# Kernel optimization log

Measured on AMD Instinct MI355X. Metric: run time of the kernel, lower is better.

The kernel has to match this reference:

```python
import jax, jax.numpy as jnp
import numpy as np
from jax import lax

# static config matching init_kwargs
H, W = 128, 128
THETA_RES, RHO_RES = 1.0, 1.0
C_IN, C_OUT = 64, 64
A = int(np.round(180.0 / THETA_RES))            # num angle bins = 180
R = int(np.ceil(np.sqrt(H * H + W * W) / RHO_RES))  # num rho bins = 182


def _make_rho_idx():
    # rho bin index for every (angle, pixel); pixels flattened h-major (h*W + w)
    th = np.arange(A, dtype=np.float64) * THETA_RES * np.pi / 180.0
    hh, ww = np.meshgrid(np.arange(H), np.arange(W), indexing='ij')
    xs = (ww - W / 2.0).ravel()
    ys = (hh - H / 2.0).ravel()
    r = np.round((xs[None, :] * np.cos(th)[:, None]
                  + ys[None, :] * np.sin(th)[:, None]) / RHO_RES).astype(np.int32)
    r = r + R // 2
    return np.clip(r, 0, R - 1)  # [A, H*W] int32


def dht(x, rho_idx):
    # Hough scatter: [N,C,H,W] -> [N,C,A,R]
    N, C, h, w = x.shape
    xf = x.reshape(N * C, h * w).T  # [HW, NC]

    def step(_, idx_a):
        acc = jax.ops.segment_sum(xf, idx_a, num_segments=R)  # [R, NC]
        return None, acc

    _, ht = lax.scan(step, None, rho_idx)       # [A, R, NC]
    return ht.transpose(2, 0, 1).reshape(N, C, A, R)


def idht(ht, rho_idx):
    # inverse Hough gather (transpose of dht): [N,C,A,R] -> [N,C,H,W]
    N, C, a, r = ht.shape
    hf = ht.reshape(N * C, a, r).transpose(1, 0, 2)  # [A, NC, R]

    def step(acc, args):
        ht_a, idx_a = args
        return acc + ht_a[:, idx_a], None  # gather along rho -> [NC, HW]

    acc0 = jnp.zeros((N * C, H * W), ht.dtype)
    acc, _ = lax.scan(step, acc0, (hf, rho_idx))
    return acc.reshape(N, C, H, W)


def conv91_relu(x, w, b, groups):
    # Conv2d kernel (9,1), padding (4,0), stride 1 + ReLU
    y = lax.conv_general_dilated(x, w, (1, 1), [(4, 4), (0, 0)],
                                 dimension_numbers=('NCHW', 'OIHW', 'NCHW'),
                                 feature_group_count=groups)
    return jax.nn.relu(y + b[None, :, None, None])


def setup_inputs():
    key = jax.random.key(0)
    ks = jax.random.split(key, 7)
    N = 4
    x = jax.random.normal(ks[0], (N, C_IN, H, W), dtype=jnp.float32)
    s1 = 1.0 / np.sqrt(9.0)
    s2 = 1.0 / np.sqrt(9.0 * C_IN)
    w1 = jax.random.normal(ks[1], (C_IN, 1, 9, 1), jnp.float32) * s1
    b1 = jax.random.normal(ks[2], (C_IN,), jnp.float32) * 0.01
    w2 = jax.random.normal(ks[3], (C_IN, C_IN, 9, 1), jnp.float32) * s2
    b2 = jax.random.normal(ks[4], (C_IN,), jnp.float32) * 0.01
    w3 = jax.random.normal(ks[5], (C_OUT, C_IN, 9, 1), jnp.float32) * s2
    b3 = jax.random.normal(ks[6], (C_OUT,), jnp.float32) * 0.01
    rho_idx = jnp.asarray(_make_rho_idx())  # [A, H*W] int32, precomputed buffer
    return {"x": x, "rho_idx": rho_idx, "w1": w1, "b1": b1,
            "w2": w2, "b2": b2, "w3": w3, "b3": b3}


def reference(x, rho_idx, w1, b1, w2, b2, w3, b3):
    out = dht(x, rho_idx)                       # [N,C,A,R]
    out = conv91_relu(out, w1, b1, groups=C_IN) # grouped (9,1) conv
    out = conv91_relu(out, w2, b2, groups=1)
    out = conv91_relu(out, w3, b3, groups=1)
    return idht(out, rho_idx)                   # [N,C_OUT,H,W]
```

## Files before the change

### kernel.cpp

```cpp
#include <hip/hip_runtime.h>

typedef unsigned short ushort_t;
typedef __attribute__((ext_vector_type(8))) short short8;
typedef __attribute__((ext_vector_type(4))) float float4v;

#define HW 16384
#define A_BINS 180
#define R_BINS 182
#define AP 188
#define CCH 64
#define NB 4
#define NC 256
#define MROWS (A_BINS * R_BINS)
#define MPROWS (AP * R_BINS)

static __device__ __forceinline__ float b2f(ushort_t u) {
    union { unsigned u32; float f; } c; c.u32 = ((unsigned)u) << 16; return c.f;
}
static __device__ __forceinline__ float u2f(unsigned u) {
    union { unsigned u32; float f; } c; c.u32 = u; return c.f;
}
static __device__ __forceinline__ ushort_t f2b(float f) {
    union { float f; unsigned u; } c; c.f = f;
    unsigned r = c.u + 0x7fffu + ((c.u >> 16) & 1u);
    return (ushort_t)(r >> 16);
}
static __device__ __forceinline__ float4v cvt4(uint2 u) {
    return (float4v){u2f(u.x << 16), u2f(u.x & 0xffff0000u),
                     u2f(u.y << 16), u2f(u.y & 0xffff0000u)};
}

__global__ __launch_bounds__(256) void k_transpose(const float* __restrict__ x,
                                                   ushort_t* __restrict__ xT) {
    __shared__ float tile[64][65];
    int t = threadIdx.x, lane = t & 63, g = t >> 6;
    int pBase = blockIdx.x * 64;
    int ncBase = blockIdx.y * 64;
#pragma unroll
    for (int i = 0; i < 16; ++i) {
        int ncl = g + i * 4;
        tile[ncl][lane] = x[(size_t)(ncBase + ncl) * HW + pBase + lane];
    }
    __syncthreads();
#pragma unroll
    for (int i = 0; i < 16; ++i) {
        int pl = g + i * 4;
        xT[(size_t)(pBase + pl) * 256 + ncBase + lane] = f2b(tile[lane][pl]);
    }
}

__global__ __launch_bounds__(256) void k_setup(ushort_t* __restrict__ ht0,
                                               ushort_t* __restrict__ bufA,
                                               ushort_t* __restrict__ bufB,
                                               const float* __restrict__ w2,
                                               const float* __restrict__ w3,
                                               ushort_t* __restrict__ w2b,
                                               ushort_t* __restrict__ w3b) {
    int blk = blockIdx.x, t = threadIdx.x;
    if (blk < 24) {
        int b = blk >> 3, j = blk & 7;
        int ap = (j < 4) ? j : (184 + (j - 4));
        ushort_t* base = (b == 0 ? ht0 : (b == 1 ? bufA : bufB));
        uint4* p = (uint4*)(base + (size_t)ap * (R_BINS * NC));
        int n16 = R_BINS * NC / 8;
        for (int i = t; i < n16; i += 256) p[i] = (uint4){0, 0, 0, 0};
        return;
    }
    int rep = blk - 24;
    const float* w = (rep >= 144) ? w3 : w2;
    ushort_t* wb = (rep >= 144) ? w3b : w2b;
    int idx = (rep % 144) * 256 + t;
    int j = idx & 7;
    int lane = (idx >> 3) & 63;
    int cot = (idx >> 9) & 3;
    int h = (idx >> 11) & 1;
    int k = idx >> 12;
    int co = cot * 16 + (lane & 15);
    int ci = h * 32 + (lane >> 4) * 8 + j;
    wb[idx] = f2b(w[(co * 64 + ci) * 9 + k]);
}

__global__ __launch_bounds__(256) void k_csr(const int* __restrict__ rho,
                                             int* __restrict__ offs,
                                             ushort_t* __restrict__ plist) {
    __shared__ int hist[4][R_BINS];
    __shared__ int tot[R_BINS];
    __shared__ int offl[R_BINS + 1];
    __shared__ int cur[4][R_BINS];
    __shared__ ushort_t sp[HW];
    int a = blockIdx.x, t = threadIdx.x, lane = t & 63, wv = t >> 6;
    for (int i = t; i < 4 * R_BINS; i += 256) ((int*)hist)[i] = 0;
    __syncthreads();
    const int* rA = rho + (size_t)a * HW;
#pragma unroll 4
    for (int i = 0; i < 64; ++i) {
        int r = rA[t + i * 256];
        atomicAdd(&hist[wv][r], 1);
    }
    __syncthreads();
    if (t < R_BINS) tot[t] = hist[0][t] + hist[1][t] + hist[2][t] + hist[3][t];
    __syncthreads();
    if (wv == 0) {
        int b0 = lane * 3;
        int c0 = (b0     < R_BINS) ? tot[b0]     : 0;
        int c1 = (b0 + 1 < R_BINS) ? tot[b0 + 1] : 0;
        int c2 = (b0 + 2 < R_BINS) ? tot[b0 + 2] : 0;
        int sum = c0 + c1 + c2, inc = sum;
#pragma unroll
        for (int d = 1; d < 64; d <<= 1) {
            int vv = __shfl_up(inc, d);
            if (lane >= d) inc += vv;
        }
        int excl = inc - sum;
        if (b0     < R_BINS) offl[b0]     = excl;
        if (b0 + 1 < R_BINS) offl[b0 + 1] = excl + c0;
        if (b0 + 2 < R_BINS) offl[b0 + 2] = excl + c0 + c1;
        if (lane == 63) offl[R_BINS] = inc;
    }
    __syncthreads();
    if (t < R_BINS) {
        int b = offl[t];
        cur[0][t] = b; b += hist[0][t];
        cur[1][t] = b; b += hist[1][t];
        cur[2][t] = b; b += hist[2][t];
        cur[3][t] = b;
    }
    if (t <= R_BINS) offs[a * (R_BINS + 1) + t] = offl[t];
    __syncthreads();
#pragma unroll 4
    for (int i = 0; i < 64; ++i) {
        int p = t + i * 256;
        int r = rA[p];
        int pos = atomicAdd(&cur[wv][r], 1);
        sp[pos] = (ushort_t)p;
    }
    __syncthreads();
    const uint4* spv = (const uint4*)sp;
    uint4* plv = (uint4*)(plist + (size_t)a * HW);
    for (int i = t; i < HW / 8; i += 256) plv[i] = spv[i];
}

__global__ __launch_bounds__(256, 4) void k_dht_g4(const ushort_t* __restrict__ xT,
                                                   const int* __restrict__ offs,
                                                   const ushort_t* __restrict__ plist,
                                                   ushort_t* __restrict__ ht0) {
    int a = blockIdx.x, part = blockIdx.y;
    int t = threadIdx.x, lane = t & 63, wv = t >> 6;
    int wslot = part * 4 + wv;
    int lo4 = lane << 2;
    const uint*  plw = (const uint*)(plist + (size_t)a * HW);
    const uint4* plq = (const uint4*)plw;
    const int* offA = offs + a * (R_BINS + 1);
    size_t obase = (size_t)(a + 4) * (R_BINS * NC);
    for (int r = wslot; r < R_BINS; r += 64) {
        int off = __builtin_amdgcn_readfirstlane(offA[r]);
        int end = __builtin_amdgcn_readfirstlane(offA[r + 1]);
        float4v acc = (float4v){0.f, 0.f, 0.f, 0.f};
        int j = off;
        while (j < end && (j & 7)) {
            unsigned up = __builtin_amdgcn_readfirstlane(plw[j >> 1]);
            unsigned p = (j & 1) ? (up >> 16) : (up & 0xffffu);
            acc += cvt4(*(const uint2*)(xT + ((size_t)p << 8) + lo4));
            ++j;
        }
        if (j + 16 <= end) {
            uint4 q0 = plq[j >> 3];
            uint4 q1 = plq[(j >> 3) + 1];
            for (; j + 16 <= end; ) {
                int jn = j + 16;
                uint4 n0, n1;
                bool more = (jn + 16 <= end);
                if (more) {
                    n0 = plq[jn >> 3];
                    n1 = plq[(jn >> 3) + 1];
                }
                unsigned w0 = __builtin_amdgcn_readfirstlane(q0.x);
                unsigned w1 = __builtin_amdgcn_readfirstlane(q0.y);
                unsigned w2 = __builtin_amdgcn_readfirstlane(q0.z);
                unsigned w3 = __builtin_amdgcn_readfirstlane(q0.w);
                unsigned w4 = __builtin_amdgcn_readfirstlane(q1.x);
                unsigned w5 = __builtin_amdgcn_readfirstlane(q1.y);
                unsigned w6 = __builtin_amdgcn_readfirstlane(q1.z);
                unsigned w7 = __builtin_amdgcn_readfirstlane(q1.w);
                uint2 u0 = *(const uint2*)(xT + ((size_t)(w0 & 0xffffu) << 8) + lo4);
                uint2 u1 = *(const uint2*)(xT + ((size_t)(w0 >> 16)     << 8) + lo4);
                uint2 u2 = *(const uint2*)(xT + ((size_t)(w1 & 0xffffu) << 8) + lo4);
                uint2 u3 = *(const uint2*)(xT + ((size_t)(w1 >> 16)     << 8) + lo4);
                uint2 u4 = *(const uint2*)(xT + ((size_t)(w2 & 0xffffu) << 8) + lo4);
                uint2 u5 = *(const uint2*)(xT + ((size_t)(w2 >> 16)     << 8) + lo4);
                uint2 u6 = *(const uint2*)(xT + ((size_t)(w3 & 0xffffu) << 8) + lo4);
                uint2 u7 = *(const uint2*)(xT + ((size_t)(w3 >> 16)     << 8) + lo4);
                uint2 u8 = *(const uint2*)(xT + ((size_t)(w4 & 0xffffu) << 8) + lo4);
                uint2 u9 = *(const uint2*)(xT + ((size_t)(w4 >> 16)     << 8) + lo4);
                uint2 ua = *(const uint2*)(xT + ((size_t)(w5 & 0xffffu) << 8) + lo4);
                uint2 ub = *(const uint2*)(xT + ((size_t)(w5 >> 16)     << 8) + lo4);
                uint2 uc = *(const uint2*)(xT + ((size_t)(w6 & 0xffffu) << 8) + lo4);
                uint2 ud = *(const uint2*)(xT + ((size_t)(w6 >> 16)     << 8) + lo4);
                uint2 ue = *(const uint2*)(xT + ((size_t)(w7 & 0xffffu) << 8) + lo4);
                uint2 uf = *(const uint2*)(xT + ((size_t)(w7 >> 16)     << 8) + lo4);
                acc += cvt4(u0); acc += cvt4(u1); acc += cvt4(u2); acc += cvt4(u3);
                acc += cvt4(u4); acc += cvt4(u5); acc += cvt4(u6); acc += cvt4(u7);
                acc += cvt4(u8); acc += cvt4(u9); acc += cvt4(ua); acc += cvt4(ub);
                acc += cvt4(uc); acc += cvt4(ud); acc += cvt4(ue); acc += cvt4(uf);
                q0 = n0; q1 = n1; j = jn;
            }
        }
        for (; j + 8 <= end; j += 8) {
            uint4 q0 = plq[j >> 3];
            unsigned w0 = __builtin_amdgcn_readfirstlane(q0.x);
            unsigned w1 = __builtin_amdgcn_readfirstlane(q0.y);
            unsigned w2 = __builtin_amdgcn_readfirstlane(q0.z);
            unsigned w3 = __builtin_amdgcn_readfirstlane(q0.w);
            uint2 u0 = *(const uint2*)(xT + ((size_t)(w0 & 0xffffu) << 8) + lo4);
            uint2 u1 = *(const uint2*)(xT + ((size_t)(w0 >> 16)     << 8) + lo4);
            uint2 u2 = *(const uint2*)(xT + ((size_t)(w1 & 0xffffu) << 8) + lo4);
            uint2 u3 = *(const uint2*)(xT + ((size_t)(w1 >> 16)     << 8) + lo4);
            uint2 u4 = *(const uint2*)(xT + ((size_t)(w2 & 0xffffu) << 8) + lo4);
            uint2 u5 = *(const uint2*)(xT + ((size_t)(w2 >> 16)     << 8) + lo4);
            uint2 u6 = *(const uint2*)(xT + ((size_t)(w3 & 0xffffu) << 8) + lo4);
            uint2 u7 = *(const uint2*)(xT + ((size_t)(w3 >> 16)     << 8) + lo4);
            acc += cvt4(u0); acc += cvt4(u1); acc += cvt4(u2); acc += cvt4(u3);
            acc += cvt4(u4); acc += cvt4(u5); acc += cvt4(u6); acc += cvt4(u7);
        }
        while (j < end) {
            unsigned up = __builtin_amdgcn_readfirstlane(plw[j >> 1]);
            unsigned p = (j & 1) ? (up >> 16) : (up & 0xffffu);
            acc += cvt4(*(const uint2*)(xT + ((size_t)p << 8) + lo4));
            ++j;
        }
        unsigned lo = (unsigned)f2b(acc.x) | ((unsigned)f2b(acc.y) << 16);
        unsigned hi = (unsigned)f2b(acc.z) | ((unsigned)f2b(acc.w) << 16);
        *(uint2*)(ht0 + obase + (size_t)r * NC + lo4) = (uint2){lo, hi};
    }
}

__global__ __launch_bounds__(256) void k_conv1(const ushort_t* __restrict__ ht0,
                                               const float* __restrict__ w1,
                                               const float* __restrict__ b1,
                                               ushort_t* __restrict__ bufA) {
    int t = threadIdx.x, c = t & 63;
    int r = blockIdx.x;
    int a0 = blockIdx.y * 30;
    float wr[9];
#pragma unroll
    for (int k = 0; k < 9; ++k) wr[k] = w1[c * 9 + k];
    float bb = b1[c];
    const ushort_t* ip = ht0 + ((size_t)a0 * R_BINS + r) * NC + t;
    float v[38];
#pragma unroll
    for (int j = 0; j < 38; ++j) v[j] = b2f(ip[(size_t)j * (R_BINS * NC)]);
    ushort_t* op = bufA + ((size_t)(a0 + 4) * R_BINS + r) * NC + t;
#pragma unroll
    for (int i = 0; i < 30; ++i) {
        float s = bb;
#pragma unroll
        for (int k = 0; k < 9; ++k) s = fmaf(v[i + k], wr[k], s);
        op[(size_t)i * (R_BINS * NC)] = f2b(fmaxf(s, 0.f));
    }
}

__global__ __launch_bounds__(256) void k_gemm(const ushort_t* __restrict__ in,
                                              const ushort_t* __restrict__ wb,
                                              const float* __restrict__ bias,
                                              ushort_t* __restrict__ out,
                                              int outRowOff) {
    __shared__ ushort_t Bs[36864];
    int t = threadIdx.x, lane = t & 63, wv = t >> 6;
    {
        const uint4* src = (const uint4*)wb;
        uint4* dst = (uint4*)Bs;
        for (int i = t; i < 36864 / 8; i += 256) dst[i] = src[i];
    }
    __syncthreads();
    int m = lane & 15, q = lane >> 4;
    int n = blockIdx.y;
    int rowBase = blockIdx.x * 256 + wv * 64;
    const ushort_t* inN = in + n * 64;
    size_t rof[4];
#pragma unroll
    for (int tl = 0; tl < 4; ++tl) {
        int row = rowBase + tl * 16 + m;
        int rowc = row < MROWS ? row : (MROWS - 1);
        rof[tl] = (size_t)rowc * NC;
    }
    float4v acc[4][4];
#pragma unroll
    for (int tl = 0; tl < 4; ++tl)
#pragma unroll
        for (int i = 0; i < 4; ++i) acc[tl][i] = (float4v){0.f, 0.f, 0.f, 0.f};

#pragma unroll
    for (int k = 0; k < 9; ++k) {
#pragma unroll
        for (int h = 0; h < 2; ++h) {
            const ushort_t* base = inN + (size_t)k * (R_BINS * NC) + h * 32 + q * 8;
            short8 af0 = *(const short8*)(base + rof[0]);
            short8 af1 = *(const short8*)(base + rof[1]);
            short8 af2 = *(const short8*)(base + rof[2]);
            short8 af3 = *(const short8*)(base + rof[3]);
            const ushort_t* bl = Bs + (size_t)((k * 2 + h) * 4) * 512 + lane * 8;
            short8 b0 = *(const short8*)(bl);
            short8 b1v = *(const short8*)(bl + 512);
            short8 b2v = *(const short8*)(bl + 1024);
            short8 b3v = *(const short8*)(bl + 1536);
            acc[0][0] = __builtin_amdgcn_mfma_f32_16x16x32_bf16(af0, b0, acc[0][0], 0, 0, 0);
            acc[0][1] = __builtin_amdgcn_mfma_f32_16x16x32_bf16(af0, b1v, acc[0][1], 0, 0, 0);
            acc[0][2] = __builtin_amdgcn_mfma_f32_16x16x32_bf16(af0, b2v, acc[0][2], 0, 0, 0);
            acc[0][3] = __builtin_amdgcn_mfma_f32_16x16x32_bf16(af0, b3v, acc[0][3], 0, 0, 0);
            acc[1][0] = __builtin_amdgcn_mfma_f32_16x16x32_bf16(af1, b0, acc[1][0], 0, 0, 0);
            acc[1][1] = __builtin_amdgcn_mfma_f32_16x16x32_bf16(af1, b1v, acc[1][1], 0, 0, 0);
            acc[1][2] = __builtin_amdgcn_mfma_f32_16x16x32_bf16(af1, b2v, acc[1][2], 0, 0, 0);
            acc[1][3] = __builtin_amdgcn_mfma_f32_16x16x32_bf16(af1, b3v, acc[1][3], 0, 0, 0);
            acc[2][0] = __builtin_amdgcn_mfma_f32_16x16x32_bf16(af2, b0, acc[2][0], 0, 0, 0);
            acc[2][1] = __builtin_amdgcn_mfma_f32_16x16x32_bf16(af2, b1v, acc[2][1], 0, 0, 0);
            acc[2][2] = __builtin_amdgcn_mfma_f32_16x16x32_bf16(af2, b2v, acc[2][2], 0, 0, 0);
            acc[2][3] = __builtin_amdgcn_mfma_f32_16x16x32_bf16(af2, b3v, acc[2][3], 0, 0, 0);
            acc[3][0] = __builtin_amdgcn_mfma_f32_16x16x32_bf16(af3, b0, acc[3][0], 0, 0, 0);
            acc[3][1] = __builtin_amdgcn_mfma_f32_16x16x32_bf16(af3, b1v, acc[3][1], 0, 0, 0);
            acc[3][2] = __builtin_amdgcn_mfma_f32_16x16x32_bf16(af3, b2v, acc[3][2], 0, 0, 0);
            acc[3][3] = __builtin_amdgcn_mfma_f32_16x16x32_bf16(af3, b3v, acc[3][3], 0, 0, 0);
        }
    }

    ushort_t* outN = out + n * 64;
#pragma unroll
    for (int tl = 0; tl < 4; ++tl) {
#pragma unroll
        for (int cot = 0; cot < 4; ++cot) {
            int co = cot * 16 + m;
            float bv = bias[co];
#pragma unroll
            for (int i = 0; i < 4; ++i) {
                int rowD = rowBase + tl * 16 + q * 4 + i;
                float v = fmaxf(acc[tl][cot][i] + bv, 0.f);
                if (rowD < MROWS) outN[(size_t)(rowD + outRowOff) * NC + co] = f2b(v);
            }
        }
    }
}

union SharedIdht {
    int rhoL[A_BINS * 32];
    float tile[2 * 256 * 33];
};

#define IDHT_LOAD(S, ang) do { \
    int4 rv0_ = *(const int4*)&u.rhoL[(ang) * 32 + wq * 8]; \
    int4 rv1_ = *(const int4*)&u.rhoL[(ang) * 32 + wq * 8 + 4]; \
    int rrs_[8] = {rv0_.x, rv0_.y, rv0_.z, rv0_.w, rv1_.x, rv1_.y, rv1_.z, rv1_.w}; \
    const ushort_t* bA_ = buf3 + (size_t)(ang) * (R_BINS * NC); \
    _Pragma("unroll") \
    for (int i_ = 0; i_ < 8; ++i_) { \
        int r_ = __builtin_amdgcn_readfirstlane(rrs_[i_]); \
        S[i_] = *(const uint2*)(bA_ + (size_t)r_ * NC + lo4); \
    } } while (0)

#define IDHT_CONSUME(S) do { \
    _Pragma("unroll") \
    for (int i_ = 0; i_ < 8; ++i_) accv[i_] += cvt4(S[i_]); \
    } while (0)

__global__ __launch_bounds__(512, 2) void k_idht(const ushort_t* __restrict__ buf3,
                                                 const int* __restrict__ rho,
                                                 float* __restrict__ outp) {
    __shared__ SharedIdht u;
    int t = threadIdx.x, lane = t & 63, wv = t >> 6;
    int grp = wv >> 2;
    int wq = wv & 3;
    int P0 = blockIdx.x * 32;
    int lo4 = lane << 2;
    for (int i = t; i < A_BINS * 32; i += 512) {
        int a = i >> 5, px = i & 31;
        u.rhoL[a * 32 + px] = rho[(size_t)a * HW + P0 + px];
    }
    __syncthreads();
    float4v accv[8];
#pragma unroll
    for (int i = 0; i < 8; ++i) accv[i] = (float4v){0.f, 0.f, 0.f, 0.f};
    int a0 = grp * 90;

    uint2 S0[8], S1[8], S2[8];
    IDHT_LOAD(S0, a0);
    IDHT_LOAD(S1, a0 + 1);
    IDHT_LOAD(S2, a0 + 2);
    for (int k = 0; k <= 84; k += 3) {
        IDHT_CONSUME(S0); IDHT_LOAD(S0, a0 + k + 3);
        IDHT_CONSUME(S1); IDHT_LOAD(S1, a0 + k + 4);
        IDHT_CONSUME(S2); IDHT_LOAD(S2, a0 + k + 5);
    }
    IDHT_CONSUME(S0);
    IDHT_CONSUME(S1);
    IDHT_CONSUME(S2);

    __syncthreads();
#pragma unroll
    for (int i = 0; i < 8; ++i) {
        int px = wq * 8 + i;
#pragma unroll
        for (int c = 0; c < 4; ++c)
            u.tile[(size_t)grp * 8448 + (lane * 4 + c) * 33 + px] = accv[i][c];
    }
    __syncthreads();
    int px = t & 31, nc0 = t >> 5;
    float* on = outp + P0 + px;
#pragma unroll
    for (int k = 0; k < 16; ++k) {
        int nc = nc0 + k * 16;
        on[(size_t)nc * HW] = u.tile[nc * 33 + px] + u.tile[8448 + nc * 33 + px];
    }
}

extern "C" void kernel_launch(void* const* d_in, const int* in_sizes, int n_in,
                              void* d_out, int out_size, void* d_ws, size_t ws_size,
                              hipStream_t stream) {
    const float* x   = (const float*)d_in[0];
    const int*   rho = (const int*)d_in[1];
    const float* w1  = (const float*)d_in[2];
    const float* b1  = (const float*)d_in[3];
    const float* w2  = (const float*)d_in[4];
    const float* b2  = (const float*)d_in[5];
    const float* w3  = (const float*)d_in[6];
    const float* b3  = (const float*)d_in[7];
    float* outp = (float*)d_out;

    char* ws = (char*)d_ws;
    size_t off = 0;
    auto alloc = [&](size_t bytes) -> void* {
        void* p = ws + off;
        off = (off + bytes + 255) & ~(size_t)255;
        return p;
    };
    ushort_t* xT    = (ushort_t*)alloc((size_t)HW * NC * 2);
    ushort_t* ht0   = (ushort_t*)alloc((size_t)AP * R_BINS * NC * 2);
    ushort_t* bufA  = (ushort_t*)alloc((size_t)AP * R_BINS * NC * 2);
    ushort_t* bufB  = (ushort_t*)alloc((size_t)AP * R_BINS * NC * 2);
    ushort_t* buf3  = (ushort_t*)alloc((size_t)A_BINS * R_BINS * NC * 2);
    ushort_t* w2b   = (ushort_t*)alloc(36864 * 2);
    ushort_t* w3b   = (ushort_t*)alloc(36864 * 2);
    int*      offs  = (int*)alloc((size_t)A_BINS * (R_BINS + 1) * 4);
    ushort_t* plist = (ushort_t*)alloc((size_t)A_BINS * HW * 2);

    k_transpose<<<dim3(256, 4), 256, 0, stream>>>(x, xT);
    k_setup<<<312, 256, 0, stream>>>(ht0, bufA, bufB, w2, w3, w2b, w3b);
    k_csr<<<A_BINS, 256, 0, stream>>>(rho, offs, plist);
    k_dht_g4<<<dim3(A_BINS, 16), 256, 0, stream>>>(xT, offs, plist, ht0);
    k_conv1<<<dim3(R_BINS, 6), 256, 0, stream>>>(ht0, w1, b1, bufA);
    k_gemm<<<dim3(128, NB), 256, 0, stream>>>(bufA, w2b, b2, bufB, 728);
    k_gemm<<<dim3(128, NB), 256, 0, stream>>>(bufB, w3b, b3, buf3, 0);
    k_idht<<<dim3(512), 512, 0, stream>>>(buf3, rho, outp);
}
```

Before: 385.0 us.

## Split DHT channel range across blocks and pixel pairs across half-wavefronts

The Hough scatter kernel now splits the 256 channels into two halves handled by separate blocks, doubling the grid. Within a wavefront, the two 32-lane halves take the even and odd pixels of each pair and combine their partial sums with a cross-half shuffle before the store. This halves the serial gather chain per wavefront and adds more blocks for latency hiding. In exchange each block reads the pixel lists twice and pays for the shuffle reduction and extra index selection.

```diff
diff --git a/kernel.cpp b/kernel.cpp
--- a/kernel.cpp
+++ b/kernel.cpp
@@ -144,24 +144,38 @@
                                                    const int* __restrict__ offs,
                                                    const ushort_t* __restrict__ plist,
                                                    ushort_t* __restrict__ ht0) {
-    int a = blockIdx.x, part = blockIdx.y;
+    int ax = blockIdx.x;
+    int a = ax >> 1, half = ax & 1;
+    int part = blockIdx.y;
     int t = threadIdx.x, lane = t & 63, wv = t >> 6;
     int wslot = part * 4 + wv;
-    int lo4 = lane << 2;
+    int lh = lane & 31;
+    bool lowhalf = (lane < 32);
+    int lh4 = lh * 4;
+    const ushort_t* xh = xT + half * 128;
     const uint*  plw = (const uint*)(plist + (size_t)a * HW);
     const uint4* plq = (const uint4*)plw;
     const int* offA = offs + a * (R_BINS + 1);
-    size_t obase = (size_t)(a + 4) * (R_BINS * NC);
+    size_t obase = (size_t)(a + 4) * (R_BINS * NC) + half * 128;
     for (int r = wslot; r < R_BINS; r += 64) {
         int off = __builtin_amdgcn_readfirstlane(offA[r]);
         int end = __builtin_amdgcn_readfirstlane(offA[r + 1]);
         float4v acc = (float4v){0.f, 0.f, 0.f, 0.f};
         int j = off;
-        while (j < end && (j & 7)) {
+        if (j < end && (j & 1)) {
             unsigned up = __builtin_amdgcn_readfirstlane(plw[j >> 1]);
-            unsigned p = (j & 1) ? (up >> 16) : (up & 0xffffu);
-            acc += cvt4(*(const uint2*)(xT + ((size_t)p << 8) + lo4));
+            unsigned p = up >> 16;
+            uint2 u = *(const uint2*)(xh + (size_t)p * 256 + lh4);
+            if (lowhalf) acc += cvt4(u);
             ++j;
+        }
+        while (j + 2 <= end && (j & 7)) {
+            unsigned w = __builtin_amdgcn_readfirstlane(plw[j >> 1]);
+            unsigned pe = w & 0xffffu, po = w >> 16;
+            unsigned ps = lowhalf ? pe : po;
+            uint2 u = *(const uint2*)(xh + (size_t)ps * 256 + lh4);
+            acc += cvt4(u);
+            j += 2;
         }
         if (j + 16 <= end) {
             uint4 q0 = plq[j >> 3];
@@ -182,55 +196,68 @@
                 unsigned w5 = __builtin_amdgcn_readfirstlane(q1.y);
                 unsigned w6 = __builtin_amdgcn_readfirstlane(q1.z);
                 unsigned w7 = __builtin_amdgcn_readfirstlane(q1.w);
-                uint2 u0 = *(const uint2*)(xT + ((size_t)(w0 & 0xffffu) << 8) + lo4);
-                uint2 u1 = *(const uint2*)(xT + ((size_t)(w0 >> 16)     << 8) + lo4);
-                uint2 u2 = *(const uint2*)(xT + ((size_t)(w1 & 0xffffu) << 8) + lo4);
-                uint2 u3 = *(const uint2*)(xT + ((size_t)(w1 >> 16)     << 8) + lo4);
-                uint2 u4 = *(const uint2*)(xT + ((size_t)(w2 & 0xffffu) << 8) + lo4);
-                uint2 u5 = *(const uint2*)(xT + ((size_t)(w2 >> 16)     << 8) + lo4);
-                uint2 u6 = *(const uint2*)(xT + ((size_t)(w3 & 0xffffu) << 8) + lo4);
-                uint2 u7 = *(const uint2*)(xT + ((size_t)(w3 >> 16)     << 8) + lo4);
-                uint2 u8 = *(const uint2*)(xT + ((size_t)(w4 & 0xffffu) << 8) + lo4);
-                uint2 u9 = *(const uint2*)(xT + ((size_t)(w4 >> 16)     << 8) + lo4);
-                uint2 ua = *(const uint2*)(xT + ((size_t)(w5 & 0xffffu) << 8) + lo4);
-                uint2 ub = *(const uint2*)(xT + ((size_t)(w5 >> 16)     << 8) + lo4);
-                uint2 uc = *(const uint2*)(xT + ((size_t)(w6 & 0xffffu) << 8) + lo4);
-                uint2 ud = *(const uint2*)(xT + ((size_t)(w6 >> 16)     << 8) + lo4);
-                uint2 ue = *(const uint2*)(xT + ((size_t)(w7 & 0xffffu) << 8) + lo4);
-                uint2 uf = *(const uint2*)(xT + ((size_t)(w7 >> 16)     << 8) + lo4);
+                unsigned s0 = lowhalf ? (w0 & 0xffffu) : (w0 >> 16);
+                unsigned s1 = lowhalf ? (w1 & 0xffffu) : (w1 >> 16);
+                unsigned s2 = lowhalf ? (w2 & 0xffffu) : (w2 >> 16);
+                unsigned s3 = lowhalf ? (w3 & 0xffffu) : (w3 >> 16);
+                unsigned s4 = lowhalf ? (w4 & 0xffffu) : (w4 >> 16);
+                unsigned s5 = lowhalf ? (w5 & 0xffffu) : (w5 >> 16);
+                unsigned s6 = lowhalf ? (w6 & 0xffffu) : (w6 >> 16);
+                unsigned s7 = lowhalf ? (w7 & 0xffffu) : (w7 >> 16);
+                uint2 u0 = *(const uint2*)(xh + (size_t)s0 * 256 + lh4);
+                uint2 u1 = *(const uint2*)(xh + (size_t)s1 * 256 + lh4);
+                uint2 u2 = *(const uint2*)(xh + (size_t)s2 * 256 + lh4);
+                uint2 u3 = *(const uint2*)(xh + (size_t)s3 * 256 + lh4);
+                uint2 u4 = *(const uint2*)(xh + (size_t)s4 * 256 + lh4);
+                uint2 u5 = *(const uint2*)(xh + (size_t)s5 * 256 + lh4);
+                uint2 u6 = *(const uint2*)(xh + (size_t)s6 * 256 + lh4);
+                uint2 u7 = *(const uint2*)(xh + (size_t)s7 * 256 + lh4);
                 acc += cvt4(u0); acc += cvt4(u1); acc += cvt4(u2); acc += cvt4(u3);
                 acc += cvt4(u4); acc += cvt4(u5); acc += cvt4(u6); acc += cvt4(u7);
-                acc += cvt4(u8); acc += cvt4(u9); acc += cvt4(ua); acc += cvt4(ub);
-                acc += cvt4(uc); acc += cvt4(ud); acc += cvt4(ue); acc += cvt4(uf);
                 q0 = n0; q1 = n1; j = jn;
             }
         }
         for (; j + 8 <= end; j += 8) {
-            uint4 q0 = plq[j >> 3];
-            unsigned w0 = __builtin_amdgcn_readfirstlane(q0.x);
-            unsigned w1 = __builtin_amdgcn_readfirstlane(q0.y);
-            unsigned w2 = __builtin_amdgcn_readfirstlane(q0.z);
-            unsigned w3 = __builtin_amdgcn_readfirstlane(q0.w);
-            uint2 u0 = *(const uint2*)(xT + ((size_t)(w0 & 0xffffu) << 8) + lo4);
-            uint2 u1 = *(const uint2*)(xT + ((size_t)(w0 >> 16)     << 8) + lo4);
-            uint2 u2 = *(const uint2*)(xT + ((size_t)(w1 & 0xffffu) << 8) + lo4);
-            uint2 u3 = *(const uint2*)(xT + ((size_t)(w1 >> 16)     << 8) + lo4);
-            uint2 u4 = *(const uint2*)(xT + ((size_t)(w2 & 0xffffu) << 8) + lo4);
-            uint2 u5 = *(const uint2*)(xT + ((size_t)(w2 >> 16)     << 8) + lo4);
-            uint2 u6 = *(const uint2*)(xT + ((size_t)(w3 & 0xffffu) << 8) + lo4);
-            uint2 u7 = *(const uint2*)(xT + ((size_t)(w3 >> 16)     << 8) + lo4);
+            uint4 q = plq[j >> 3];
+            unsigned w0 = __builtin_amdgcn_readfirstlane(q.x);
+            unsigned w1 = __builtin_amdgcn_readfirstlane(q.y);
+            unsigned w2 = __builtin_amdgcn_readfirstlane(q.z);
+            unsigned w3 = __builtin_amdgcn_readfirstlane(q.w);
+            unsigned s0 = lowhalf ? (w0 & 0xffffu) : (w0 >> 16);
+            unsigned s1 = lowhalf ? (w1 & 0xffffu) : (w1 >> 16);
+            unsigned s2 = lowhalf ? (w2 & 0xffffu) : (w2 >> 16);
+            unsigned s3 = lowhalf ? (w3 & 0xffffu) : (w3 >> 16);
+            uint2 u0 = *(const uint2*)(xh + (size_t)s0 * 256 + lh4);
+            uint2 u1 = *(const uint2*)(xh + (size_t)s1 * 256 + lh4);
+            uint2 u2 = *(const uint2*)(xh + (size_t)s2 * 256 + lh4);
+            uint2 u3 = *(const uint2*)(xh + (size_t)s3 * 256 + lh4);
             acc += cvt4(u0); acc += cvt4(u1); acc += cvt4(u2); acc += cvt4(u3);
-            acc += cvt4(u4); acc += cvt4(u5); acc += cvt4(u6); acc += cvt4(u7);
-        }
-        while (j < end) {
+        }
+        while (j + 2 <= end) {
+            unsigned w = __builtin_amdgcn_readfirstlane(plw[j >> 1]);
+            unsigned pe = w & 0xffffu, po = w >> 16;
+            unsigned ps = lowhalf ? pe : po;
+            uint2 u = *(const uint2*)(xh + (size_t)ps * 256 + lh4);
+            acc += cvt4(u);
+            j += 2;
+        }
+        if (j < end) {
             unsigned up = __builtin_amdgcn_readfirstlane(plw[j >> 1]);
-            unsigned p = (j & 1) ? (up >> 16) : (up & 0xffffu);
-            acc += cvt4(*(const uint2*)(xT + ((size_t)p << 8) + lo4));
-            ++j;
-        }
-        unsigned lo = (unsigned)f2b(acc.x) | ((unsigned)f2b(acc.y) << 16);
-        unsigned hi = (unsigned)f2b(acc.z) | ((unsigned)f2b(acc.w) << 16);
-        *(uint2*)(ht0 + obase + (size_t)r * NC + lo4) = (uint2){lo, hi};
+            unsigned p = up & 0xffffu;
+            uint2 u = *(const uint2*)(xh + (size_t)p * 256 + lh4);
+            if (lowhalf) acc += cvt4(u);
+        }
+        float4v oth;
+        oth.x = __shfl(acc.x, lane ^ 32);
+        oth.y = __shfl(acc.y, lane ^ 32);
+        oth.z = __shfl(acc.z, lane ^ 32);
+        oth.w = __shfl(acc.w, lane ^ 32);
+        acc += oth;
+        if (lowhalf) {
+            unsigned lo = (unsigned)f2b(acc.x) | ((unsigned)f2b(acc.y) << 16);
+            unsigned hi = (unsigned)f2b(acc.z) | ((unsigned)f2b(acc.w) << 16);
+            *(uint2*)(ht0 + obase + (size_t)r * NC + lh4) = (uint2){lo, hi};
+        }
     }
 }
 
@@ -443,7 +470,7 @@
     k_transpose<<<dim3(256, 4), 256, 0, stream>>>(x, xT);
     k_setup<<<312, 256, 0, stream>>>(ht0, bufA, bufB, w2, w3, w2b, w3b);
     k_csr<<<A_BINS, 256, 0, stream>>>(rho, offs, plist);
-    k_dht_g4<<<dim3(A_BINS, 16), 256, 0, stream>>>(xT, offs, plist, ht0);
+    k_dht_g4<<<dim3(360, 16), 256, 0, stream>>>(xT, offs, plist, ht0);
     k_conv1<<<dim3(R_BINS, 6), 256, 0, stream>>>(ht0, w1, b1, bufA);
     k_gemm<<<dim3(128, NB), 256, 0, stream>>>(bufA, w2b, b2, bufB, 728);
     k_gemm<<<dim3(128, NB), 256, 0, stream>>>(bufB, w3b, b3, buf3, 0);
```

Result: faster. 373.9 us (-2.9%).
